# Performance work log

Measured on AMD Instinct MI355X. Metric: run time of the kernel, lower is better.

The kernel has to match this reference:

```python
import jax, jax.numpy as jnp
import numpy as np

N, E, B, K = 100000, 3200000, 500, 30
F_IN, H1, NUM_CLASSES = 128, 64, 18


def _gcn_conv(x, W, b, row, col, w_edge, n_nodes):
    # PyG GCNConv: remove_self_loops happened outside (w_edge=0 on self loops),
    # GCNConv re-adds self loops -> deg = in_deg + 1, norm = d^-1/2[row]*d^-1/2[col].
    xw = x @ W
    deg = jax.ops.segment_sum(w_edge, col, num_segments=n_nodes) + 1.0
    dis = jax.lax.rsqrt(deg)
    coef = dis[row] * dis[col] * w_edge           # [E]
    msg = xw[row] * coef[:, None]                 # [E, C] irregular gather
    agg = jax.ops.segment_sum(msg, col, num_segments=n_nodes)
    agg = agg + xw * (dis * dis)[:, None]         # self-loop term
    return agg + b


def _sort_pool(x, batch, num_graphs, k):
    # SortAggregation: per-graph sort descending by last channel, keep top-k, zero-pad.
    n, c = x.shape
    score = x[:, -1]
    perm = jnp.lexsort((-score, batch))           # sort by (batch asc, score desc)
    b_sorted = batch[perm]
    counts = jax.ops.segment_sum(jnp.ones((n,), x.dtype), batch, num_segments=num_graphs)
    starts = jnp.cumsum(counts) - counts          # segment start offsets
    pos = jnp.arange(n) - starts[b_sorted].astype(jnp.int32)
    pos = jnp.where(pos < k, pos, k)              # out-of-range -> dropped
    out = jnp.zeros((num_graphs, k, c), x.dtype).at[b_sorted, pos].set(x[perm], mode='drop')
    return out.reshape(num_graphs, k * c)


def _conv1d(x, w, b, stride):
    y = jax.lax.conv_general_dilated(x, w, (stride,), 'VALID',
                                     dimension_numbers=('NCH', 'OIH', 'NCH'))
    return y + b[None, :, None]


def setup_inputs() -> dict:
    key = jax.random.key(0)
    ks = jax.random.split(key, 16)
    x = jax.random.normal(ks[0], (N, F_IN), dtype=jnp.float32)
    edge_index = jax.random.randint(ks[1], (2, E), 0, N, dtype=jnp.int32)
    batch = jnp.sort(jax.random.randint(ks[2], (N,), 0, B, dtype=jnp.int32))
    s = 0.05
    return {
        'x': x, 'edge_index': edge_index, 'batch': batch, 'num_graphs': B,
        'W1': jax.random.normal(ks[3], (F_IN, H1), jnp.float32) * s,
        'b1': jnp.zeros((H1,), jnp.float32),
        'W2': jax.random.normal(ks[4], (H1, 1), jnp.float32) * s,
        'b2': jnp.zeros((1,), jnp.float32),
        'conv3_w': jax.random.normal(ks[5], (16, 1, 97), jnp.float32) * s,
        'conv3_b': jnp.zeros((16,), jnp.float32),
        'conv4_w': jax.random.normal(ks[6], (32, 16, 5), jnp.float32) * s,
        'conv4_b': jnp.zeros((32,), jnp.float32),
        'fc1_w': jax.random.normal(ks[7], (192, 128), jnp.float32) * s,
        'fc1_b': jnp.zeros((128,), jnp.float32),
        'fc2_w': jax.random.normal(ks[8], (128, NUM_CLASSES), jnp.float32) * s,
        'fc2_b': jnp.zeros((NUM_CLASSES,), jnp.float32),
    }


def reference(x, edge_index, batch, num_graphs, W1, b1, W2, b2,
              conv3_w, conv3_b, conv4_w, conv4_b, fc1_w, fc1_b, fc2_w, fc2_b):
    row, col = edge_index[0], edge_index[1]
    w_edge = (row != col).astype(x.dtype)         # remove_self_loops
    x1 = jnp.tanh(_gcn_conv(x, W1, b1, row, col, w_edge, x.shape[0]))   # [N,64]
    x2 = jnp.tanh(_gcn_conv(x1, W2, b2, row, col, w_edge, x.shape[0]))  # [N,1]
    xc = jnp.concatenate([x1, x2], axis=-1)       # [N,65]
    p = _sort_pool(xc, batch, num_graphs, K)      # [B, 1950]
    h = p[:, None, :]                             # [B,1,1950]
    h = jax.nn.relu(_conv1d(h, conv3_w, conv3_b, 97))                   # [B,16,20]
    h = jax.lax.reduce_window(h, -jnp.inf, jax.lax.max,
                              (1, 1, 2), (1, 1, 2), 'VALID')            # [B,16,10]
    h = jax.nn.relu(_conv1d(h, conv4_w, conv4_b, 1))                    # [B,32,6]
    h = h.reshape(h.shape[0], -1)                 # [B,192]
    last_layer = jax.nn.relu(h @ fc1_w + fc1_b)   # [B,128] (dropout = eval identity)
    out = last_layer @ fc2_w + fc2_b              # [B,18]
    classes = jax.nn.log_softmax(out, axis=-1)
    return (classes, out, last_layer)
```

## Files before the change

kernel.cpp:

```cpp
#include <hip/hip_runtime.h>
#include <math.h>

#define N_NODES 100000
#define N_EDGES 3200000
#define B_GRAPHS 500
#define K_TOP 30
#define F_INN 128
#define H1C 64
#define NUM_CLASSES 18
#define XC 65
#define P_LEN (K_TOP * XC)
#define C3_OUT 16
#define C3_K 97
#define C3_L 20
#define P2_L 10
#define C4_OUT 32
#define C4_K 5
#define C4_L 6
#define FC1_IN 192
#define FC1_OUT 128

#define BK_SHIFT 7
#define BK_NODES 128
#define NBKT ((N_NODES + BK_NODES - 1) / BK_NODES)
#define BSTRIDE 5120
#define MS_EPT 32
#define MS_EPB (256 * MS_EPT)

#define REG_B 544

typedef __attribute__((ext_vector_type(8))) short bf16x8;
typedef __attribute__((ext_vector_type(4))) float f32x4;
typedef __attribute__((ext_vector_type(2))) unsigned int u32x2;

static __device__ __forceinline__ unsigned short f2bf(float f) {
    unsigned int u = __float_as_uint(f);
    u += 0x7FFFu + ((u >> 16) & 1u);
    return (unsigned short)(u >> 16);
}

__global__ __launch_bounds__(256) void k_mscatter(const int* __restrict__ row,
                                                  const int* __restrict__ col,
                                                  int* __restrict__ gcur,
                                                  unsigned int* __restrict__ ebkt) {
    __shared__ int hist[NBKT];
    __shared__ int base[NBKT];
    int tid = threadIdx.x;
    for (int i = tid; i < NBKT; i += 256) hist[i] = 0;
    __syncthreads();
    unsigned int pk[MS_EPT];
    unsigned int pay[MS_EPT];
    int e0 = blockIdx.x * MS_EPB;
#pragma unroll
    for (int j = 0; j < MS_EPT; ++j) {
        int e = e0 + j * 256 + tid;
        pk[j] = 0xFFFFFFFFu;
        if (e < N_EDGES) {
            int r = row[e], c = col[e];
            if (r != c) {
                int b = c >> BK_SHIFT;
                int rank = atomicAdd(&hist[b], 1);
                pk[j] = ((unsigned int)b << 12) | (unsigned int)rank;
                pay[j] = ((unsigned int)r << BK_SHIFT) | (unsigned int)(c & (BK_NODES - 1));
            }
        }
    }
    __syncthreads();
    for (int i = tid; i < NBKT; i += 256)
        base[i] = hist[i] ? (i * BSTRIDE + atomicAdd(&gcur[i], hist[i])) : 0;
    __syncthreads();
#pragma unroll
    for (int j = 0; j < MS_EPT; ++j) {
        if (pk[j] != 0xFFFFFFFFu) {
            int b = pk[j] >> 12;
            int rank = pk[j] & 0xFFF;
            ebkt[base[b] + rank] = pay[j];
        }
    }
}

__global__ __launch_bounds__(256) void k_csr(const unsigned int* __restrict__ ebkt,
                                             const int* __restrict__ gcur,
                                             float* __restrict__ dis,
                                             int2* __restrict__ rowse,
                                             int* __restrict__ erow) {
    __shared__ unsigned int ebs[BSTRIDE];
    __shared__ int cnt[BK_NODES];
    __shared__ int s[256];
    __shared__ int cur[BK_NODES];
    int b = blockIdx.x, t = threadIdx.x;
    if (t < BK_NODES) cnt[t] = 0;
    __syncthreads();
    int n = gcur[b];
    int lo = b * BSTRIDE;
    for (int i = t; i < n; i += 256) {
        unsigned int pk = ebkt[lo + i];
        ebs[i] = pk;
        atomicAdd(&cnt[pk & (BK_NODES - 1)], 1);
    }
    __syncthreads();
    int v = (t < BK_NODES) ? cnt[t] : 0;
    s[t] = v;
    __syncthreads();
    for (int off = 1; off < BK_NODES; off <<= 1) {
        int add = (t >= off) ? s[t - off] : 0;
        __syncthreads();
        s[t] += add;
        __syncthreads();
    }
    int ex = s[t] - v;
    if (t < BK_NODES) {
        int node = b * BK_NODES + t;
        if (node < N_NODES) {
            dis[node] = rsqrtf((float)v + 1.0f);
            rowse[node] = make_int2(lo + ex, lo + ex + v);
        }
        cur[t] = lo + ex;
    }
    __syncthreads();
    for (int i = t; i < n; i += 256) {
        unsigned int pk = ebs[i];
        int cl = pk & (BK_NODES - 1);
        int slot = atomicAdd(&cur[cl], 1);
        erow[slot] = (int)((pk >> BK_SHIFT) << 7);
    }
}

__global__ __launch_bounds__(256) void k_xw1(const float* __restrict__ x,
                                             const float* __restrict__ W1,
                                             const float* __restrict__ dis,
                                             unsigned short* __restrict__ xw) {
    __shared__ unsigned short w1s[16 * 64 * 8];
    int tid = threadIdx.x;
    if (blockIdx.x == 0 && tid < 32)
        ((unsigned int*)(xw + (size_t)N_NODES * H1C))[tid] = 0;
    for (int idx = tid; idx < 16 * 64 * 8; idx += 256) {
        int f = idx >> 9;
        int l = (idx >> 3) & 63;
        int j = idx & 7;
        int kq = f >> 2, t4 = f & 3;
        int k = kq * 32 + ((l >> 4) << 3) + j;
        int n = t4 * 16 + (l & 15);
        w1s[idx] = f2bf(W1[k * H1C + n]);
    }
    __syncthreads();
    int wave = tid >> 6;
    int lane = tid & 63;
    int quad = lane >> 4;
    int m = lane & 15;
    int wrow0 = blockIdx.x * 256 + wave * 64;

    bf16x8 bw[16];
#pragma unroll
    for (int f = 0; f < 16; ++f)
        bw[f] = *(const bf16x8*)&w1s[(f * 64 + lane) * 8];

#pragma unroll
    for (int rt = 0; rt < 4; ++rt) {
        int trow0 = wrow0 + rt * 16;
        f32x4 acc[4];
#pragma unroll
        for (int t = 0; t < 4; ++t) acc[t] = (f32x4){0.f, 0.f, 0.f, 0.f};

        int rowA = trow0 + m;
        size_t ra = (size_t)(rowA < N_NODES ? rowA : N_NODES - 1);
#pragma unroll
        for (int kq = 0; kq < 4; ++kq) {
            const float* xp = x + ra * F_INN + kq * 32 + quad * 8;
            float4 f0 = ((const float4*)xp)[0];
            float4 f1 = ((const float4*)xp)[1];
            bf16x8 a;
            a[0] = (short)f2bf(f0.x); a[1] = (short)f2bf(f0.y);
            a[2] = (short)f2bf(f0.z); a[3] = (short)f2bf(f0.w);
            a[4] = (short)f2bf(f1.x); a[5] = (short)f2bf(f1.y);
            a[6] = (short)f2bf(f1.z); a[7] = (short)f2bf(f1.w);
#pragma unroll
            for (int t = 0; t < 4; ++t)
                acc[t] = __builtin_amdgcn_mfma_f32_16x16x32_bf16(a, bw[kq * 4 + t], acc[t], 0, 0, 0);
        }
#pragma unroll
        for (int r = 0; r < 4; ++r) {
            int rowD = trow0 + quad * 4 + r;
            if (rowD < N_NODES) {
                float dsc = dis[rowD];
#pragma unroll
                for (int t = 0; t < 4; ++t)
                    xw[(size_t)rowD * H1C + t * 16 + m] = f2bf(acc[t][r] * dsc);
            }
        }
    }
}

__global__ __launch_bounds__(256) void k_agg1m(const int2* __restrict__ rowse,
                                               const int* __restrict__ erow,
                                               const unsigned short* __restrict__ xws,
                                               const float* __restrict__ dis,
                                               const float* __restrict__ b1,
                                               const float* __restrict__ W2,
                                               float* __restrict__ x1,
                                               float* __restrict__ xws2) {
    __shared__ __align__(16) char slds[4][8 * REG_B];
    int tid = threadIdx.x;
    int wave = tid >> 6;
    int lane = tid & 63;
    int wid = blockIdx.x * 4 + wave;
    int grp = lane >> 3;
    int sub = lane & 7;
    int2 se = rowse[wid];
    int base = se.x, endp = se.y;
    int nE = endp - base;
    const char* xb = (const char*)xws;
    const int ZR = N_NODES << 7;

    char* wreg = &slds[wave][0];
    char* dst0 = wreg + ((sub >> 1) * 2 + ((grp >> 2) & 1)) * REG_B + (grp & 3) * 32 + (sub & 1) * 16;
    unsigned int trb = (unsigned int)(size_t)wreg +
                       (unsigned int)(((lane >> 4) * 64 + (lane & 15)) * 2);

    bf16x8 aones;
#pragma unroll
    for (int i = 0; i < 8; ++i) aones[i] = (short)0x3F80;

    f32x4 ac0 = (f32x4){0.f, 0.f, 0.f, 0.f};
    f32x4 ac1 = ac0, ac2 = ac0, ac3 = ac0;

    for (int w0 = 0; w0 < nE; w0 += 64) {
        int idx = base + w0 + lane;
        int myoff = (idx < endp) ? erow[idx] : ZR;
#pragma unroll
        for (int hf = 0; hf < 2; ++hf) {
            if (w0 + hf * 32 < nE) {
#pragma unroll
                for (int ii = 0; ii < 4; ++ii) {
                    int o = __shfl(myoff, hf * 32 + ii * 8 + grp);
                    uint4 v = ((const uint4*)(xb + o))[sub];
                    *(uint4*)(dst0 + ii * 128) = v;
                }
                asm volatile("s_waitcnt lgkmcnt(0)" ::: "memory");
                __builtin_amdgcn_sched_barrier(0);
                u32x2 q0, q1, q2, q3, q4, q5, q6, q7;
                asm volatile("ds_read_b64_tr_b16 %0, %1 offset:0"    : "=v"(q0) : "v"(trb) : "memory");
                asm volatile("ds_read_b64_tr_b16 %0, %1 offset:544"  : "=v"(q1) : "v"(trb) : "memory");
                asm volatile("ds_read_b64_tr_b16 %0, %1 offset:1088" : "=v"(q2) : "v"(trb) : "memory");
                asm volatile("ds_read_b64_tr_b16 %0, %1 offset:1632" : "=v"(q3) : "v"(trb) : "memory");
                asm volatile("ds_read_b64_tr_b16 %0, %1 offset:2176" : "=v"(q4) : "v"(trb) : "memory");
                asm volatile("ds_read_b64_tr_b16 %0, %1 offset:2720" : "=v"(q5) : "v"(trb) : "memory");
                asm volatile("ds_read_b64_tr_b16 %0, %1 offset:3264" : "=v"(q6) : "v"(trb) : "memory");
                asm volatile("ds_read_b64_tr_b16 %0, %1 offset:3808" : "=v"(q7) : "v"(trb) : "memory");
                asm volatile("s_waitcnt lgkmcnt(0)" ::: "memory");
                __builtin_amdgcn_sched_barrier(0);
                union FU { bf16x8 f; unsigned int d[4]; };
                FU f0, f1, f2, f3;
                f0.d[0] = q0.x; f0.d[1] = q0.y; f0.d[2] = q1.x; f0.d[3] = q1.y;
                f1.d[0] = q2.x; f1.d[1] = q2.y; f1.d[2] = q3.x; f1.d[3] = q3.y;
                f2.d[0] = q4.x; f2.d[1] = q4.y; f2.d[2] = q5.x; f2.d[3] = q5.y;
                f3.d[0] = q6.x; f3.d[1] = q6.y; f3.d[2] = q7.x; f3.d[3] = q7.y;
                ac0 = __builtin_amdgcn_mfma_f32_16x16x32_bf16(aones, f0.f, ac0, 0, 0, 0);
                ac1 = __builtin_amdgcn_mfma_f32_16x16x32_bf16(aones, f1.f, ac1, 0, 0, 0);
                ac2 = __builtin_amdgcn_mfma_f32_16x16x32_bf16(aones, f2.f, ac2, 0, 0, 0);
                ac3 = __builtin_amdgcn_mfma_f32_16x16x32_bf16(aones, f3.f, ac3, 0, 0, 0);
            }
        }
    }
    float v0 = __shfl(ac0[0], lane & 15);
    float v1 = __shfl(ac1[0], lane & 15);
    float v2 = __shfl(ac2[0], lane & 15);
    float v3 = __shfl(ac3[0], lane & 15);
    int ts = lane >> 4;
    float aggv = ts == 0 ? v0 : (ts == 1 ? v1 : (ts == 2 ? v2 : v3));
    float d = dis[wid];
    unsigned int su = xws[(size_t)wid * H1C + lane];
    float self = __uint_as_float(su << 16);
    float v = tanhf(d * (aggv + self) + b1[lane]);
    x1[(size_t)wid * H1C + lane] = v;
    float s = v * W2[lane];
#pragma unroll
    for (int off = 1; off < 64; off <<= 1) s += __shfl_xor(s, off);
    if (lane == 0) xws2[wid] = d * s;
}

__global__ __launch_bounds__(256) void k_x2(const int2* __restrict__ rowse,
                                            const int* __restrict__ erow,
                                            const float* __restrict__ xws2,
                                            const float* __restrict__ dis,
                                            const float* __restrict__ b2,
                                            float* __restrict__ x2) {
    int lane = threadIdx.x & 63;
    int wglob = (blockIdx.x * 256 + threadIdx.x) >> 6;
    int grp = lane >> 3;
    int sub = lane & 7;
    int node = wglob * 8 + grp;
    int2 se = rowse[node];
    float acc = 0.0f;
    for (int i = se.x + sub; i < se.y; i += 8)
        acc += xws2[erow[i] >> 7];
    acc += __shfl_xor(acc, 1);
    acc += __shfl_xor(acc, 2);
    acc += __shfl_xor(acc, 4);
    if (sub == 0)
        x2[node] = tanhf(dis[node] * (acc + xws2[node]) + b2[0]);
}

__global__ __launch_bounds__(256) void k_poolhead(const int* __restrict__ batch,
                                                  const float* __restrict__ x1,
                                                  const float* __restrict__ x2,
                                                  const float* __restrict__ w3, const float* __restrict__ b3,
                                                  const float* __restrict__ w4, const float* __restrict__ b4,
                                                  const float* __restrict__ fw1, const float* __restrict__ fb1,
                                                  const float* __restrict__ fw2, const float* __restrict__ fb2,
                                                  float* __restrict__ out) {
    __shared__ float x2s[512];
    __shared__ int sel[K_TOP];
    __shared__ float ps[P_LEN];
    __shared__ float h1s[C3_OUT * C3_L];
    __shared__ float h2s[C3_OUT * P2_L];
    __shared__ float h3s[FC1_IN];
    __shared__ float lls[FC1_OUT];
    __shared__ float outs[NUM_CLASSES];
    int g = blockIdx.x, tid = threadIdx.x;
    int lo = 0, hi = N_NODES;
    while (lo < hi) { int m = (lo + hi) >> 1; if (batch[m] < g) lo = m + 1; else hi = m; }
    int start = lo;
    hi = N_NODES;
    while (lo < hi) { int m = (lo + hi) >> 1; if (batch[m] < g + 1) lo = m + 1; else hi = m; }
    int end = lo;
    int count = end - start;
    if (count > 512) count = 512;
    for (int t = tid; t < count; t += 256) x2s[t] = x2[start + t];
    __syncthreads();
    int wave = tid >> 6, lane = tid & 63;
    if (wave == 0) {
        unsigned long long k[8];
#pragma unroll
        for (int i = 0; i < 8; ++i) {
            int idx = i * 64 + lane;
            unsigned long long key = 0ULL;
            if (idx < count) {
                unsigned int bits = __float_as_uint(x2s[idx]);
                unsigned int u = (bits & 0x80000000u) ? ~bits : (bits | 0x80000000u);
                key = ((unsigned long long)u << 32) | (unsigned int)(~(unsigned int)(start + idx));
            }
            k[i] = key;
        }
        int kk = count < K_TOP ? count : K_TOP;
        for (int j = 0; j < kk; ++j) {
            unsigned long long best = k[0];
#pragma unroll
            for (int i = 1; i < 8; ++i) if (k[i] > best) best = k[i];
#pragma unroll
            for (int off = 32; off; off >>= 1) {
                unsigned long long o = __shfl_xor(best, off);
                if (o > best) best = o;
            }
            int node = (int)(~(unsigned int)(best & 0xFFFFFFFFULL));
#pragma unroll
            for (int i = 0; i < 8; ++i) if (k[i] == best) k[i] = 0ULL;
            if (lane == 0) sel[j] = node;
        }
        if (lane >= kk && lane < K_TOP) sel[lane] = -1;
    }
    __syncthreads();
    for (int t = tid; t < P_LEN; t += 256) {
        int j = t / XC, c = t - j * XC;
        int node = sel[j];
        float v = 0.0f;
        if (node >= 0) v = (c < H1C) ? x1[(size_t)node * H1C + c] : x2s[node - start];
        ps[t] = v;
    }
    __syncthreads();
    for (int o = tid; o < C3_OUT * C3_L; o += 256) {
        int oc = o / C3_L, pos = o % C3_L;
        float s = b3[oc];
        const float* w = w3 + oc * C3_K;
        int base = pos * C3_K;
        for (int k = 0; k < C3_K; ++k) s += ps[base + k] * w[k];
        h1s[o] = fmaxf(s, 0.0f);
    }
    __syncthreads();
    if (tid < C3_OUT * P2_L) {
        int oc = tid / P2_L, pos = tid % P2_L;
        h2s[tid] = fmaxf(h1s[oc * C3_L + 2 * pos], h1s[oc * C3_L + 2 * pos + 1]);
    }
    __syncthreads();
    if (tid < C4_OUT * C4_L) {
        int oc = tid / C4_L, pos = tid % C4_L;
        float s = b4[oc];
        for (int ic = 0; ic < C3_OUT; ++ic)
#pragma unroll
            for (int k = 0; k < C4_K; ++k)
                s += h2s[ic * P2_L + pos + k] * w4[oc * C3_OUT * C4_K + ic * C4_K + k];
        h3s[oc * C4_L + pos] = fmaxf(s, 0.0f);
    }
    __syncthreads();
    if (tid < FC1_OUT) {
        float s = fb1[tid];
        for (int i = 0; i < FC1_IN; ++i) s += h3s[i] * fw1[i * FC1_OUT + tid];
        float v = fmaxf(s, 0.0f);
        lls[tid] = v;
        out[2 * B_GRAPHS * NUM_CLASSES + (size_t)g * FC1_OUT + tid] = v;
    }
    __syncthreads();
    if (tid < NUM_CLASSES) {
        float s = fb2[tid];
        for (int j = 0; j < FC1_OUT; ++j) s += lls[j] * fw2[j * NUM_CLASSES + tid];
        outs[tid] = s;
        out[B_GRAPHS * NUM_CLASSES + (size_t)g * NUM_CLASSES + tid] = s;
    }
    __syncthreads();
    if (tid < NUM_CLASSES) {
        float m = -INFINITY;
        for (int k2 = 0; k2 < NUM_CLASSES; ++k2) m = fmaxf(m, outs[k2]);
        float se = 0.0f;
        for (int k2 = 0; k2 < NUM_CLASSES; ++k2) se += expf(outs[k2] - m);
        out[(size_t)g * NUM_CLASSES + tid] = outs[tid] - m - logf(se);
    }
}

extern "C" void kernel_launch(void* const* d_in, const int* in_sizes, int n_in,
                              void* d_out, int out_size, void* d_ws, size_t ws_size,
                              hipStream_t stream) {
    const float* x   = (const float*)d_in[0];
    const int*   ei  = (const int*)d_in[1];
    const int*   row = ei;
    const int*   col = ei + N_EDGES;
    const int*   bat = (const int*)d_in[2];
    const float* W1  = (const float*)d_in[4];
    const float* b1  = (const float*)d_in[5];
    const float* W2  = (const float*)d_in[6];
    const float* b2  = (const float*)d_in[7];
    const float* w3  = (const float*)d_in[8];
    const float* b3  = (const float*)d_in[9];
    const float* w4  = (const float*)d_in[10];
    const float* b4  = (const float*)d_in[11];
    const float* fw1 = (const float*)d_in[12];
    const float* fb1 = (const float*)d_in[13];
    const float* fw2 = (const float*)d_in[14];
    const float* fb2 = (const float*)d_in[15];

    char* wsb = (char*)d_ws;
    unsigned short* xws = (unsigned short*)wsb;       wsb += (size_t)(N_NODES + 1) * H1C * 2;
    float* x1     = (float*)wsb;                      wsb += (size_t)N_NODES * H1C * 4;
    int*   erow   = (int*)wsb;                        wsb += (size_t)NBKT * BSTRIDE * 4;
    unsigned int* ebkt = (unsigned int*)x1;
    int*   gcur   = (int*)wsb;                        wsb += (size_t)NBKT * 4;
    int2*  rowse  = (int2*)wsb;                       wsb += (size_t)N_NODES * 8;
    float* dis    = (float*)wsb;                      wsb += (size_t)N_NODES * 4;
    float* xws2   = (float*)wsb;                      wsb += (size_t)N_NODES * 4;
    float* x2     = (float*)wsb;                      wsb += (size_t)N_NODES * 4;
    float* outp   = (float*)d_out;

    hipMemsetAsync(gcur, 0, (size_t)NBKT * 4, stream);

    k_mscatter<<<(N_EDGES + MS_EPB - 1) / MS_EPB, 256, 0, stream>>>(row, col, gcur, ebkt);
    k_csr<<<NBKT, 256, 0, stream>>>(ebkt, gcur, dis, rowse, erow);
    k_xw1<<<(N_NODES + 255) / 256, 256, 0, stream>>>(x, W1, dis, xws);
    k_agg1m<<<N_NODES / 4, 256, 0, stream>>>(rowse, erow, xws, dis, b1, W2, x1, xws2);
    k_x2<<<N_NODES / (8 * 4), 256, 0, stream>>>(rowse, erow, xws2, dis, b2, x2);
    k_poolhead<<<B_GRAPHS, 256, 0, stream>>>(bat, x1, x2,
                                             w3, b3, w4, b4, fw1, fb1, fw2, fb2, outp);
}
```

Before: 317.8 us.

## Merge memset, edge scatter, CSR build and XW1 into one cooperative kernel

Replaces the memset plus three front kernels (bucket scatter, per-bucket CSR build, X·W1 MFMA) with a single cooperative kernel of NBKT blocks that uses grid.sync between phases. Shared memory is reused across phases, and the edge scatter now reads row and col as int4 with 4096 edges per block. The aim is to remove launch gaps and the memset. In exchange it pays for grid-wide barriers and needs all 782 blocks to be co-resident (launch bounds 256,4), and the scatter's work per block is smaller.

```diff
diff --git a/kernel.cpp b/kernel.cpp
--- a/kernel.cpp
+++ b/kernel.cpp
@@ -1,5 +1,8 @@
 #include <hip/hip_runtime.h>
+#include <hip/hip_cooperative_groups.h>
 #include <math.h>
+
+namespace cg = cooperative_groups;
 
 #define N_NODES 100000
 #define N_EDGES 3200000
@@ -24,8 +27,6 @@
 #define BK_NODES 128
 #define NBKT ((N_NODES + BK_NODES - 1) / BK_NODES)
 #define BSTRIDE 5120
-#define MS_EPT 32
-#define MS_EPB (256 * MS_EPT)
 
 #define REG_B 544
 
@@ -39,153 +40,167 @@
     return (unsigned short)(u >> 16);
 }
 
-__global__ __launch_bounds__(256) void k_mscatter(const int* __restrict__ row,
+__global__ __launch_bounds__(256, 4) void k_front(const int* __restrict__ row,
                                                   const int* __restrict__ col,
                                                   int* __restrict__ gcur,
-                                                  unsigned int* __restrict__ ebkt) {
-    __shared__ int hist[NBKT];
-    __shared__ int base[NBKT];
-    int tid = threadIdx.x;
-    for (int i = tid; i < NBKT; i += 256) hist[i] = 0;
-    __syncthreads();
-    unsigned int pk[MS_EPT];
-    unsigned int pay[MS_EPT];
-    int e0 = blockIdx.x * MS_EPB;
-#pragma unroll
-    for (int j = 0; j < MS_EPT; ++j) {
-        int e = e0 + j * 256 + tid;
-        pk[j] = 0xFFFFFFFFu;
-        if (e < N_EDGES) {
-            int r = row[e], c = col[e];
-            if (r != c) {
-                int b = c >> BK_SHIFT;
-                int rank = atomicAdd(&hist[b], 1);
-                pk[j] = ((unsigned int)b << 12) | (unsigned int)rank;
-                pay[j] = ((unsigned int)r << BK_SHIFT) | (unsigned int)(c & (BK_NODES - 1));
-            }
-        }
-    }
-    __syncthreads();
-    for (int i = tid; i < NBKT; i += 256)
-        base[i] = hist[i] ? (i * BSTRIDE + atomicAdd(&gcur[i], hist[i])) : 0;
-    __syncthreads();
-#pragma unroll
-    for (int j = 0; j < MS_EPT; ++j) {
-        if (pk[j] != 0xFFFFFFFFu) {
-            int b = pk[j] >> 12;
-            int rank = pk[j] & 0xFFF;
-            ebkt[base[b] + rank] = pay[j];
-        }
-    }
-}
-
-__global__ __launch_bounds__(256) void k_csr(const unsigned int* __restrict__ ebkt,
-                                             const int* __restrict__ gcur,
-                                             float* __restrict__ dis,
-                                             int2* __restrict__ rowse,
-                                             int* __restrict__ erow) {
-    __shared__ unsigned int ebs[BSTRIDE];
+                                                  unsigned int* __restrict__ ebkt,
+                                                  const float* __restrict__ x,
+                                                  const float* __restrict__ W1,
+                                                  float* __restrict__ dis,
+                                                  int2* __restrict__ rowse,
+                                                  int* __restrict__ erow,
+                                                  unsigned short* __restrict__ xw) {
+    cg::grid_group grid = cg::this_grid();
+    __shared__ __align__(16) char ubuf[BSTRIDE * 4];
     __shared__ int cnt[BK_NODES];
     __shared__ int s[256];
     __shared__ int cur[BK_NODES];
-    int b = blockIdx.x, t = threadIdx.x;
-    if (t < BK_NODES) cnt[t] = 0;
-    __syncthreads();
-    int n = gcur[b];
-    int lo = b * BSTRIDE;
-    for (int i = t; i < n; i += 256) {
-        unsigned int pk = ebkt[lo + i];
-        ebs[i] = pk;
-        atomicAdd(&cnt[pk & (BK_NODES - 1)], 1);
-    }
-    __syncthreads();
-    int v = (t < BK_NODES) ? cnt[t] : 0;
-    s[t] = v;
-    __syncthreads();
-    for (int off = 1; off < BK_NODES; off <<= 1) {
-        int add = (t >= off) ? s[t - off] : 0;
-        __syncthreads();
-        s[t] += add;
-        __syncthreads();
-    }
-    int ex = s[t] - v;
-    if (t < BK_NODES) {
-        int node = b * BK_NODES + t;
-        if (node < N_NODES) {
-            dis[node] = rsqrtf((float)v + 1.0f);
-            rowse[node] = make_int2(lo + ex, lo + ex + v);
-        }
-        cur[t] = lo + ex;
-    }
-    __syncthreads();
-    for (int i = t; i < n; i += 256) {
-        unsigned int pk = ebs[i];
-        int cl = pk & (BK_NODES - 1);
-        int slot = atomicAdd(&cur[cl], 1);
-        erow[slot] = (int)((pk >> BK_SHIFT) << 7);
-    }
-}
-
-__global__ __launch_bounds__(256) void k_xw1(const float* __restrict__ x,
-                                             const float* __restrict__ W1,
-                                             const float* __restrict__ dis,
-                                             unsigned short* __restrict__ xw) {
-    __shared__ unsigned short w1s[16 * 64 * 8];
     int tid = threadIdx.x;
-    if (blockIdx.x == 0 && tid < 32)
-        ((unsigned int*)(xw + (size_t)N_NODES * H1C))[tid] = 0;
-    for (int idx = tid; idx < 16 * 64 * 8; idx += 256) {
-        int f = idx >> 9;
-        int l = (idx >> 3) & 63;
-        int j = idx & 7;
-        int kq = f >> 2, t4 = f & 3;
-        int k = kq * 32 + ((l >> 4) << 3) + j;
-        int n = t4 * 16 + (l & 15);
-        w1s[idx] = f2bf(W1[k * H1C + n]);
-    }
-    __syncthreads();
-    int wave = tid >> 6;
-    int lane = tid & 63;
-    int quad = lane >> 4;
-    int m = lane & 15;
-    int wrow0 = blockIdx.x * 256 + wave * 64;
-
-    bf16x8 bw[16];
-#pragma unroll
-    for (int f = 0; f < 16; ++f)
-        bw[f] = *(const bf16x8*)&w1s[(f * 64 + lane) * 8];
-
-#pragma unroll
-    for (int rt = 0; rt < 4; ++rt) {
-        int trow0 = wrow0 + rt * 16;
-        f32x4 acc[4];
-#pragma unroll
-        for (int t = 0; t < 4; ++t) acc[t] = (f32x4){0.f, 0.f, 0.f, 0.f};
-
-        int rowA = trow0 + m;
-        size_t ra = (size_t)(rowA < N_NODES ? rowA : N_NODES - 1);
-#pragma unroll
-        for (int kq = 0; kq < 4; ++kq) {
-            const float* xp = x + ra * F_INN + kq * 32 + quad * 8;
-            float4 f0 = ((const float4*)xp)[0];
-            float4 f1 = ((const float4*)xp)[1];
-            bf16x8 a;
-            a[0] = (short)f2bf(f0.x); a[1] = (short)f2bf(f0.y);
-            a[2] = (short)f2bf(f0.z); a[3] = (short)f2bf(f0.w);
-            a[4] = (short)f2bf(f1.x); a[5] = (short)f2bf(f1.y);
-            a[6] = (short)f2bf(f1.z); a[7] = (short)f2bf(f1.w);
-#pragma unroll
-            for (int t = 0; t < 4; ++t)
-                acc[t] = __builtin_amdgcn_mfma_f32_16x16x32_bf16(a, bw[kq * 4 + t], acc[t], 0, 0, 0);
-        }
-#pragma unroll
-        for (int r = 0; r < 4; ++r) {
-            int rowD = trow0 + quad * 4 + r;
-            if (rowD < N_NODES) {
-                float dsc = dis[rowD];
+    int b = blockIdx.x;
+
+    int gt = b * 256 + tid;
+    if (gt < NBKT) gcur[gt] = 0;
+    grid.sync();
+
+    {
+        int* hist = (int*)ubuf;
+        int* base = hist + NBKT;
+        for (int i = tid; i < NBKT; i += 256) hist[i] = 0;
+        __syncthreads();
+        unsigned int pk[16];
+        unsigned int pay[16];
+        int e0q = b * 1024;
+#pragma unroll
+        for (int j = 0; j < 4; ++j) {
+            int q = e0q + j * 256 + tid;
+            bool ok = (q * 4) < N_EDGES;
+            int4 r4 = ok ? ((const int4*)row)[q] : make_int4(0, 0, 0, 0);
+            int4 c4 = ok ? ((const int4*)col)[q] : make_int4(0, 0, 0, 0);
+#pragma unroll
+            for (int k = 0; k < 4; ++k) {
+                int jj = j * 4 + k;
+                pk[jj] = 0xFFFFFFFFu;
+                int r = k == 0 ? r4.x : k == 1 ? r4.y : k == 2 ? r4.z : r4.w;
+                int c = k == 0 ? c4.x : k == 1 ? c4.y : k == 2 ? c4.z : c4.w;
+                if (ok && r != c) {
+                    int bk = c >> BK_SHIFT;
+                    int rank = atomicAdd(&hist[bk], 1);
+                    pk[jj] = ((unsigned int)bk << 12) | (unsigned int)rank;
+                    pay[jj] = ((unsigned int)r << BK_SHIFT) | (unsigned int)(c & (BK_NODES - 1));
+                }
+            }
+        }
+        __syncthreads();
+        for (int i = tid; i < NBKT; i += 256)
+            base[i] = hist[i] ? (i * BSTRIDE + atomicAdd(&gcur[i], hist[i])) : 0;
+        __syncthreads();
+#pragma unroll
+        for (int j = 0; j < 16; ++j) {
+            if (pk[j] != 0xFFFFFFFFu) {
+                int bk = pk[j] >> 12;
+                int rank = pk[j] & 0xFFF;
+                ebkt[base[bk] + rank] = pay[j];
+            }
+        }
+    }
+    grid.sync();
+
+    {
+        unsigned int* ebs = (unsigned int*)ubuf;
+        if (tid < BK_NODES) cnt[tid] = 0;
+        __syncthreads();
+        int n = gcur[b];
+        int lo = b * BSTRIDE;
+        for (int i = tid; i < n; i += 256) {
+            unsigned int pk = ebkt[lo + i];
+            ebs[i] = pk;
+            atomicAdd(&cnt[pk & (BK_NODES - 1)], 1);
+        }
+        __syncthreads();
+        int v = (tid < BK_NODES) ? cnt[tid] : 0;
+        s[tid] = v;
+        __syncthreads();
+        for (int off = 1; off < BK_NODES; off <<= 1) {
+            int add = (tid >= off) ? s[tid - off] : 0;
+            __syncthreads();
+            s[tid] += add;
+            __syncthreads();
+        }
+        int ex = s[tid] - v;
+        if (tid < BK_NODES) {
+            int node = b * BK_NODES + tid;
+            if (node < N_NODES) {
+                dis[node] = rsqrtf((float)v + 1.0f);
+                rowse[node] = make_int2(lo + ex, lo + ex + v);
+            }
+            cur[tid] = lo + ex;
+        }
+        __syncthreads();
+        for (int i = tid; i < n; i += 256) {
+            unsigned int pk = ebs[i];
+            int cl = pk & (BK_NODES - 1);
+            int slot = atomicAdd(&cur[cl], 1);
+            erow[slot] = (int)((pk >> BK_SHIFT) << 7);
+        }
+    }
+    grid.sync();
+
+    {
+        unsigned short* w1s = (unsigned short*)ubuf;
+        if (b == 0 && tid < 32)
+            ((unsigned int*)(xw + (size_t)N_NODES * H1C))[tid] = 0;
+        for (int idx = tid; idx < 16 * 64 * 8; idx += 256) {
+            int f = idx >> 9;
+            int l = (idx >> 3) & 63;
+            int j = idx & 7;
+            int kq = f >> 2, t4 = f & 3;
+            int k = kq * 32 + ((l >> 4) << 3) + j;
+            int n = t4 * 16 + (l & 15);
+            w1s[idx] = f2bf(W1[k * H1C + n]);
+        }
+        __syncthreads();
+        int wave = tid >> 6;
+        int lane = tid & 63;
+        int quad = lane >> 4;
+        int m = lane & 15;
+
+        bf16x8 bw[16];
+#pragma unroll
+        for (int f = 0; f < 16; ++f)
+            bw[f] = *(const bf16x8*)&w1s[(f * 64 + lane) * 8];
+
+#pragma unroll
+        for (int rt = 0; rt < 2; ++rt) {
+            int wrow0 = b * 128 + rt * 64 + wave * 16;
+            f32x4 acc[4];
+#pragma unroll
+            for (int t = 0; t < 4; ++t) acc[t] = (f32x4){0.f, 0.f, 0.f, 0.f};
+
+            int rowA = wrow0 + m;
+            size_t ra = (size_t)(rowA < N_NODES ? rowA : N_NODES - 1);
+#pragma unroll
+            for (int kq = 0; kq < 4; ++kq) {
+                const float* xp = x + ra * F_INN + kq * 32 + quad * 8;
+                float4 f0 = ((const float4*)xp)[0];
+                float4 f1 = ((const float4*)xp)[1];
+                bf16x8 a;
+                a[0] = (short)f2bf(f0.x); a[1] = (short)f2bf(f0.y);
+                a[2] = (short)f2bf(f0.z); a[3] = (short)f2bf(f0.w);
+                a[4] = (short)f2bf(f1.x); a[5] = (short)f2bf(f1.y);
+                a[6] = (short)f2bf(f1.z); a[7] = (short)f2bf(f1.w);
 #pragma unroll
                 for (int t = 0; t < 4; ++t)
-                    xw[(size_t)rowD * H1C + t * 16 + m] = f2bf(acc[t][r] * dsc);
+                    acc[t] = __builtin_amdgcn_mfma_f32_16x16x32_bf16(a, bw[kq * 4 + t], acc[t], 0, 0, 0);
+            }
+#pragma unroll
+            for (int r = 0; r < 4; ++r) {
+                int rowD = wrow0 + quad * 4 + r;
+                if (rowD < N_NODES) {
+                    float dsc = dis[rowD];
+#pragma unroll
+                    for (int t = 0; t < 4; ++t)
+                        xw[(size_t)rowD * H1C + t * 16 + m] = f2bf(acc[t][r] * dsc);
+                }
             }
         }
     }
@@ -262,12 +277,12 @@
             }
         }
     }
-    float v0 = __shfl(ac0[0], lane & 15);
-    float v1 = __shfl(ac1[0], lane & 15);
-    float v2 = __shfl(ac2[0], lane & 15);
-    float v3 = __shfl(ac3[0], lane & 15);
+    float v0s = __shfl(ac0[0], lane & 15);
+    float v1s = __shfl(ac1[0], lane & 15);
+    float v2s = __shfl(ac2[0], lane & 15);
+    float v3s = __shfl(ac3[0], lane & 15);
     int ts = lane >> 4;
-    float aggv = ts == 0 ? v0 : (ts == 1 ? v1 : (ts == 2 ? v2 : v3));
+    float aggv = ts == 0 ? v0s : (ts == 1 ? v1s : (ts == 2 ? v2s : v3s));
     float d = dis[wid];
     unsigned int su = xws[(size_t)wid * H1C + lane];
     float self = __uint_as_float(su << 16);
@@ -449,11 +464,11 @@
     float* x2     = (float*)wsb;                      wsb += (size_t)N_NODES * 4;
     float* outp   = (float*)d_out;
 
-    hipMemsetAsync(gcur, 0, (size_t)NBKT * 4, stream);
-
-    k_mscatter<<<(N_EDGES + MS_EPB - 1) / MS_EPB, 256, 0, stream>>>(row, col, gcur, ebkt);
-    k_csr<<<NBKT, 256, 0, stream>>>(ebkt, gcur, dis, rowse, erow);
-    k_xw1<<<(N_NODES + 255) / 256, 256, 0, stream>>>(x, W1, dis, xws);
+    void* fargs[] = { (void*)&row, (void*)&col, (void*)&gcur, (void*)&ebkt,
+                      (void*)&x, (void*)&W1, (void*)&dis, (void*)&rowse,
+                      (void*)&erow, (void*)&xws };
+    hipLaunchCooperativeKernel((void*)k_front, dim3(NBKT), dim3(256), fargs, 0, stream);
+
     k_agg1m<<<N_NODES / 4, 256, 0, stream>>>(rowse, erow, xws, dis, b1, W2, x1, xws2);
     k_x2<<<N_NODES / (8 * 4), 256, 0, stream>>>(rowse, erow, xws2, dis, b2, x2);
     k_poolhead<<<B_GRAPHS, 256, 0, stream>>>(bat, x1, x2,
```

Result: slower. 618.6 us (+94.7%).
